# Performance work log

Hardware: AMD Instinct MI355X
Metric: run time of the kernel (lower is better)

## Reference

```python
import jax, jax.numpy as jnp
import numpy as np

B, S, D, O = 8, 2048, 1024, 1024  # batch, seq_len, state_dim(=input_dim), output_dim


def setup_inputs() -> dict:
    key = jax.random.key(0)
    k_in, k_a, k_bc = jax.random.split(key, 3)
    inputs = jax.random.normal(k_in, (B, S, D), dtype=jnp.float32)
    # Stable diagonal transition (|A| < 1) so the 2048-step recurrence stays bounded.
    A = jax.random.uniform(k_a, (D,), minval=-0.99, maxval=0.99, dtype=jnp.float32)
    BC = jax.random.normal(k_bc, (D, O), dtype=jnp.float32) / D
    return {"inputs": inputs, "A": A, "BC": BC}


def reference(inputs, A, BC):
    # Diagonal LTI recurrence: h_t = A * h_{t-1} + x_t ; out_t = h_t @ BC
    # h0 = zeros (the module's h0 Parameter is initialized to zeros).
    x_tfirst = jnp.swapaxes(inputs, 0, 1)  # [S, B, D]

    def step(h, x_t):
        h = h * A + x_t
        return h, h

    h0 = jnp.zeros((inputs.shape[0], A.shape[0]), dtype=inputs.dtype)
    _, hs = jax.lax.scan(step, h0, x_tfirst)  # hs: [S, B, D]
    # Single fused projection over all timesteps instead of per-step matmuls.
    out = jnp.einsum('sbd,do->bso', hs, BC)  # [B, S, O]
    return out
```

## Files before the change

kernel.cpp:

```cpp
#include <hip/hip_runtime.h>
#include <hip/hip_bf16.h>

#define BB 8
#define SS 2048
#define DD 1024
#define OO 1024
#define MM (BB * SS)
#define KK DD
#define NN OO
#define CC 64
#define LL 32

typedef __bf16 bf16x8 __attribute__((ext_vector_type(8)));
typedef __bf16 bf16x4 __attribute__((ext_vector_type(4)));
typedef float floatx4 __attribute__((ext_vector_type(4)));

__device__ __forceinline__ float4 fma4(float4 h, float4 a, float4 v) {
    h.x = fmaf(h.x, a.x, v.x);
    h.y = fmaf(h.y, a.y, v.y);
    h.z = fmaf(h.z, a.z, v.z);
    h.w = fmaf(h.w, a.w, v.w);
    return h;
}

__global__ __launch_bounds__(256) void prep(const float* __restrict__ x,
                                            const float* __restrict__ A,
                                            float* __restrict__ carry,
                                            const float* __restrict__ BC,
                                            __bf16* __restrict__ BCt) {
    __shared__ float tile[32][33];
    const int id = blockIdx.x;
    if (id < BB * CC) {
        const int c = id & (CC - 1);
        const int b = id >> 6;
        const int i4 = threadIdx.x;
        const float4 a = ((const float4*)A)[i4];
        const float4* xp = (const float4*)(x + ((size_t)b * SS + (size_t)c * LL) * DD) + i4;
        float4 h = make_float4(0.f, 0.f, 0.f, 0.f);
#pragma unroll
        for (int t0 = 0; t0 < LL; t0 += 8) {
            float4 v[8];
#pragma unroll
            for (int u = 0; u < 8; ++u) v[u] = xp[(size_t)(t0 + u) * (DD / 4)];
#pragma unroll
            for (int u = 0; u < 8; ++u) h = fma4(h, a, v[u]);
        }
        ((float4*)carry)[((size_t)b * CC + c) * (DD / 4) + i4] = h;
    } else {
        const int t = id - BB * CC;
        const int o0 = (t & 31) * 32;
        const int d0 = (t >> 5) * 32;
        const int tx = threadIdx.x & 31;
        const int ty = threadIdx.x >> 5;
#pragma unroll
        for (int i = 0; i < 4; ++i) {
            const int dd = ty + i * 8;
            tile[dd][tx] = BC[(size_t)(d0 + dd) * OO + o0 + tx];
        }
        __syncthreads();
#pragma unroll
        for (int i = 0; i < 4; ++i) {
            const int oo = ty + i * 8;
            BCt[(size_t)(o0 + oo) * DD + d0 + tx] = (__bf16)tile[tx][oo];
        }
    }
}

__global__ __launch_bounds__(256) void scan_emit(const float* __restrict__ x,
                                                 const float* __restrict__ A,
                                                 const float* __restrict__ carry,
                                                 __bf16* __restrict__ hs) {
    const int id = blockIdx.x;
    const int c = id & (CC - 1);
    const int b = id >> 6;
    const int i4 = threadIdx.x;
    const float4 a = ((const float4*)A)[i4];
    float4 aL = a;
#pragma unroll
    for (int i = 0; i < 5; ++i) { aL.x *= aL.x; aL.y *= aL.y; aL.z *= aL.z; aL.w *= aL.w; }
    float4 h = make_float4(0.f, 0.f, 0.f, 0.f);
    const float4* cp = (const float4*)carry + (size_t)b * CC * (DD / 4) + i4;
    for (int j = 0; j < c; ++j) {
        const float4 cv = cp[(size_t)j * (DD / 4)];
        h.x = fmaf(h.x, aL.x, cv.x);
        h.y = fmaf(h.y, aL.y, cv.y);
        h.z = fmaf(h.z, aL.z, cv.z);
        h.w = fmaf(h.w, aL.w, cv.w);
    }
    const size_t base = ((size_t)b * SS + (size_t)c * LL) * DD;
    const float4* xp = (const float4*)(x + base) + i4;
    bf16x4* hp = (bf16x4*)(hs + base) + i4;
#pragma unroll
    for (int t0 = 0; t0 < LL; t0 += 8) {
        float4 v[8];
#pragma unroll
        for (int u = 0; u < 8; ++u) v[u] = xp[(size_t)(t0 + u) * (DD / 4)];
#pragma unroll
        for (int u = 0; u < 8; ++u) {
            h = fma4(h, a, v[u]);
            bf16x4 o;
            o[0] = (__bf16)h.x; o[1] = (__bf16)h.y; o[2] = (__bf16)h.z; o[3] = (__bf16)h.w;
            hp[(size_t)(t0 + u) * (DD / 4)] = o;
        }
    }
}

#define GTM 256
#define GTN 256
#define GTK 64
#define GNT (KK / GTK)

__device__ __forceinline__ void async16(void* lds, const void* g) {
    __builtin_amdgcn_global_load_lds(
        (__attribute__((address_space(1))) void*)(void*)g,
        (__attribute__((address_space(3))) void*)lds, 16, 0, 0);
}

#define MEMFENCE asm volatile("" ::: "memory")
#define BARRIER do { MEMFENCE; __builtin_amdgcn_s_barrier(); MEMFENCE; } while (0)

__global__ __launch_bounds__(512, 2) void gemm_bt(const __bf16* __restrict__ Am,
                                                  const __bf16* __restrict__ Bt,
                                                  float* __restrict__ C) {
    __shared__ __align__(16) __bf16 As[2][GTM * GTK];
    __shared__ __align__(16) __bf16 Bs[2][GTN * GTK];

    const int tid = threadIdx.x;
    const int wave = tid >> 6;
    const int lane = tid & 63;
    const int wm = (wave >> 2) * 128;
    const int wn = (wave & 3) * 64;
    const int lanelo = lane & 15;
    const int quad = lane >> 4;

    const int bid = blockIdx.x;
    const int xcd = bid & 7;
    const int loc = bid >> 3;
    const int tile_m = (xcd * 8 + (loc >> 2)) * GTM;
    const int tile_n = (loc & 3) * GTN;

    const __bf16* Abp[4];
    const __bf16* Bbp[4];
#pragma unroll
    for (int j = 0; j < 4; ++j) {
        const int cid = tid + j * 512;
        const int r = cid >> 3;
        const int qg = ((cid & 7) ^ (r & 7)) * 8;
        Abp[j] = Am + (size_t)(tile_m + r) * KK + qg;
        Bbp[j] = Bt + (size_t)(tile_n + r) * KK + qg;
    }

    floatx4 acc[8][4];
#pragma unroll
    for (int i = 0; i < 8; ++i)
#pragma unroll
        for (int j = 0; j < 4; ++j) acc[i][j] = (floatx4){0.f, 0.f, 0.f, 0.f};

    auto stage = [&](int t, int u) {
        const int k = t * GTK;
#pragma unroll
        for (int j = 0; j < 4; ++j)
            async16(&As[u][(tid + j * 512) * 8], Abp[j] + k);
#pragma unroll
        for (int j = 0; j < 4; ++j)
            async16(&Bs[u][(tid + j * 512) * 8], Bbp[j] + k);
    };

    auto compute = [&](int u) {
        const __bf16* as = As[u];
        const __bf16* bs = Bs[u];
#pragma unroll
        for (int kk = 0; kk < 2; ++kk) {
            bf16x8 af[8], bv[4];
#pragma unroll
            for (int ii = 0; ii < 8; ++ii) {
                const int row = wm + ii * 16 + lanelo;
                af[ii] = *(const bf16x8*)(as + row * GTK + ((((kk << 2) | quad) ^ (lanelo & 7)) * 8));
            }
#pragma unroll
            for (int j = 0; j < 4; ++j) {
                const int row = wn + j * 16 + lanelo;
                bv[j] = *(const bf16x8*)(bs + row * GTK + ((((kk << 2) | quad) ^ (lanelo & 7)) * 8));
            }
            __builtin_amdgcn_s_setprio(1);
#pragma unroll
            for (int ii = 0; ii < 8; ++ii)
#pragma unroll
                for (int j = 0; j < 4; ++j)
                    acc[ii][j] = __builtin_amdgcn_mfma_f32_16x16x32_bf16(af[ii], bv[j], acc[ii][j], 0, 0, 0);
            __builtin_amdgcn_s_setprio(0);
        }
    };

    stage(0, 0);

    for (int t = 0; t < GNT - 1; ++t) {
        stage(t + 1, (t + 1) & 1);
        asm volatile("s_waitcnt vmcnt(8)" ::: "memory");
        BARRIER;
        compute(t & 1);
        BARRIER;
    }
    asm volatile("s_waitcnt vmcnt(0)" ::: "memory");
    BARRIER;
    compute((GNT - 1) & 1);

#pragma unroll
    for (int i = 0; i < 8; ++i) {
        const int row = tile_m + wm + i * 16 + quad * 4;
#pragma unroll
        for (int r = 0; r < 4; ++r) {
            float* crow = C + (size_t)(row + r) * NN + tile_n + wn + lanelo;
#pragma unroll
            for (int j = 0; j < 4; ++j) crow[j * 16] = acc[i][j][r];
        }
    }
}

extern "C" void kernel_launch(void* const* d_in, const int* in_sizes, int n_in,
                              void* d_out, int out_size, void* d_ws, size_t ws_size,
                              hipStream_t stream) {
    const float* x  = (const float*)d_in[0];
    const float* A  = (const float*)d_in[1];
    const float* BC = (const float*)d_in[2];
    float* out = (float*)d_out;

    char* ws = (char*)d_ws;
    __bf16* hs   = (__bf16*)ws;
    float* carry = (float*)(ws + 33554432);
    __bf16* BCt  = (__bf16*)(ws + 33554432 + 2097152);

    prep<<<dim3(BB * CC + 1024), 256, 0, stream>>>(x, A, carry, BC, BCt);
    scan_emit<<<dim3(BB * CC), 256, 0, stream>>>(x, A, carry, hs);
    gemm_bt<<<dim3(256), 512, 0, stream>>>(hs, BCt, out);
}
```

Baseline: 167.5 us.

## Split GEMM k-step into four quadrant phases with interleaved async loads

Restructures the bf16 GEMM main loop into four sub-phases, one per quadrant of each wave's output tile. Each phase issues a quarter of the next tile's global-to-LDS loads interleaved with LDS fragment reads and MFMAs, so memory traffic spreads across the compute rather than arriving in one burst. The LDS layout is permuted so each quarter of the staged data lines up with one quadrant, and register fragments are reused between phases. The cost is more barriers per k-step, and the vmcnt bookkeeping must be exact for the shared buffers to stay consistent.

```diff
diff --git a/kernel.cpp b/kernel.cpp
--- a/kernel.cpp
+++ b/kernel.cpp
@@ -118,6 +118,8 @@
 
 #define MEMFENCE asm volatile("" ::: "memory")
 #define BARRIER do { MEMFENCE; __builtin_amdgcn_s_barrier(); MEMFENCE; } while (0)
+#define VMCNT4 asm volatile("s_waitcnt vmcnt(4)" ::: "memory")
+#define VMCNT0 asm volatile("s_waitcnt vmcnt(0)" ::: "memory")
 
 __global__ __launch_bounds__(512, 2) void gemm_bt(const __bf16* __restrict__ Am,
                                                   const __bf16* __restrict__ Bt,
@@ -139,16 +141,39 @@
     const int tile_m = (xcd * 8 + (loc >> 2)) * GTM;
     const int tile_n = (loc & 3) * GTN;
 
-    const __bf16* Abp[4];
-    const __bf16* Bbp[4];
-#pragma unroll
-    for (int j = 0; j < 4; ++j) {
-        const int cid = tid + j * 512;
-        const int r = cid >> 3;
-        const int qg = ((cid & 7) ^ (r & 7)) * 8;
-        Abp[j] = Am + (size_t)(tile_m + r) * KK + qg;
-        Bbp[j] = Bt + (size_t)(tile_n + r) * KK + qg;
-    }
+    const __bf16* gsrc[4][2];
+    int ldsoff[4][2];
+#pragma unroll
+    for (int a = 0; a < 2; ++a)
+#pragma unroll
+        for (int u = 0; u < 2; ++u) {
+            const int idx = a * 1024 + u * 512 + tid;
+            const int rho = idx >> 3, qs = idx & 7;
+            const int rl = rho & 127;
+            const int r = (rl >> 6) * 128 + a * 64 + (rl & 63);
+            const int qg = qs ^ (rho & 7);
+            gsrc[a * 3][u] = Am + (size_t)(tile_m + r) * KK + qg * 8;
+            ldsoff[a * 3][u] = idx * 8;
+        }
+#pragma unroll
+    for (int b = 0; b < 2; ++b)
+#pragma unroll
+        for (int u = 0; u < 2; ++u) {
+            const int idx = b * 1024 + u * 512 + tid;
+            const int rho = idx >> 3, qs = idx & 7;
+            const int rl = rho & 127;
+            const int r = (rl >> 5) * 64 + b * 32 + (rl & 31);
+            const int qg = qs ^ (rho & 7);
+            gsrc[1 + b][u] = Bt + (size_t)(tile_n + r) * KK + qg * 8;
+            ldsoff[1 + b][u] = idx * 8;
+        }
+
+    auto stage = [&](int p, int bufi, int koff) {
+        __bf16* base = (p == 0 || p == 3) ? As[bufi] : Bs[bufi];
+#pragma unroll
+        for (int u = 0; u < 2; ++u)
+            async16(base + ldsoff[p][u], gsrc[p][u] + koff);
+    };
 
     floatx4 acc[8][4];
 #pragma unroll
@@ -156,54 +181,95 @@
 #pragma unroll
         for (int j = 0; j < 4; ++j) acc[i][j] = (floatx4){0.f, 0.f, 0.f, 0.f};
 
-    auto stage = [&](int t, int u) {
-        const int k = t * GTK;
-#pragma unroll
-        for (int j = 0; j < 4; ++j)
-            async16(&As[u][(tid + j * 512) * 8], Abp[j] + k);
-#pragma unroll
-        for (int j = 0; j < 4; ++j)
-            async16(&Bs[u][(tid + j * 512) * 8], Bbp[j] + k);
+    bf16x8 af[4][2];
+    bf16x8 bv[2][2][2];
+
+    auto read_a = [&](const __bf16* as, int mh) {
+#pragma unroll
+        for (int il = 0; il < 4; ++il)
+#pragma unroll
+            for (int kk = 0; kk < 2; ++kk) {
+                const int rho = mh * 128 + (wm >> 1) + il * 16 + lanelo;
+                af[il][kk] = *(const bf16x8*)(as + rho * 64 + (((kk * 4 + quad) ^ (lanelo & 7)) * 8));
+            }
     };
-
-    auto compute = [&](int u) {
-        const __bf16* as = As[u];
-        const __bf16* bs = Bs[u];
-#pragma unroll
-        for (int kk = 0; kk < 2; ++kk) {
-            bf16x8 af[8], bv[4];
-#pragma unroll
-            for (int ii = 0; ii < 8; ++ii) {
-                const int row = wm + ii * 16 + lanelo;
-                af[ii] = *(const bf16x8*)(as + row * GTK + ((((kk << 2) | quad) ^ (lanelo & 7)) * 8));
+    auto read_b = [&](const __bf16* bs, int nh) {
+#pragma unroll
+        for (int jl = 0; jl < 2; ++jl)
+#pragma unroll
+            for (int kk = 0; kk < 2; ++kk) {
+                const int rho = nh * 128 + (wn >> 1) + jl * 16 + lanelo;
+                bv[nh][jl][kk] = *(const bf16x8*)(bs + rho * 64 + (((kk * 4 + quad) ^ (lanelo & 7)) * 8));
             }
-#pragma unroll
-            for (int j = 0; j < 4; ++j) {
-                const int row = wn + j * 16 + lanelo;
-                bv[j] = *(const bf16x8*)(bs + row * GTK + ((((kk << 2) | quad) ^ (lanelo & 7)) * 8));
-            }
-            __builtin_amdgcn_s_setprio(1);
-#pragma unroll
-            for (int ii = 0; ii < 8; ++ii)
-#pragma unroll
-                for (int j = 0; j < 4; ++j)
-                    acc[ii][j] = __builtin_amdgcn_mfma_f32_16x16x32_bf16(af[ii], bv[j], acc[ii][j], 0, 0, 0);
-            __builtin_amdgcn_s_setprio(0);
-        }
     };
-
-    stage(0, 0);
+    auto mfma16 = [&](int mh, int nh) {
+        __builtin_amdgcn_s_setprio(1);
+#pragma unroll
+        for (int il = 0; il < 4; ++il)
+#pragma unroll
+            for (int jl = 0; jl < 2; ++jl)
+#pragma unroll
+                for (int kk = 0; kk < 2; ++kk)
+                    acc[mh * 4 + il][nh * 2 + jl] = __builtin_amdgcn_mfma_f32_16x16x32_bf16(
+                        af[il][kk], bv[nh][jl][kk], acc[mh * 4 + il][nh * 2 + jl], 0, 0, 0);
+        __builtin_amdgcn_s_setprio(0);
+    };
+
+    stage(0, 0, 0);
+    stage(1, 0, 0);
+    stage(2, 0, 0);
+    stage(3, 0, 0);
+    VMCNT4;
+    BARRIER;
 
     for (int t = 0; t < GNT - 1; ++t) {
-        stage(t + 1, (t + 1) & 1);
-        asm volatile("s_waitcnt vmcnt(8)" ::: "memory");
-        BARRIER;
-        compute(t & 1);
-        BARRIER;
-    }
-    asm volatile("s_waitcnt vmcnt(0)" ::: "memory");
-    BARRIER;
-    compute((GNT - 1) & 1);
+        const int cur = t & 1, nxt = cur ^ 1;
+        const __bf16* as = As[cur];
+        const __bf16* bs = Bs[cur];
+        const int ko = (t + 1) * GTK;
+
+        read_a(as, 0);
+        read_b(bs, 0);
+        stage(0, nxt, ko);
+        VMCNT4;
+        BARRIER;
+        mfma16(0, 0);
+        BARRIER;
+
+        read_b(bs, 1);
+        stage(1, nxt, ko);
+        VMCNT4;
+        BARRIER;
+        mfma16(0, 1);
+        BARRIER;
+
+        read_a(as, 1);
+        stage(2, nxt, ko);
+        BARRIER;
+        mfma16(1, 1);
+        BARRIER;
+
+        stage(3, nxt, ko);
+        VMCNT4;
+        BARRIER;
+        mfma16(1, 0);
+        BARRIER;
+    }
+
+    {
+        const __bf16* as = As[(GNT - 1) & 1];
+        const __bf16* bs = Bs[(GNT - 1) & 1];
+        VMCNT0;
+        BARRIER;
+        read_a(as, 0);
+        read_b(bs, 0);
+        mfma16(0, 0);
+        read_b(bs, 1);
+        mfma16(0, 1);
+        read_a(as, 1);
+        mfma16(1, 1);
+        mfma16(1, 0);
+    }
 
 #pragma unroll
     for (int i = 0; i < 8; ++i) {
```

Result: no change. 167.7 us (+0.1%).
